# Kernel tuning notes

Hardware: AMD Instinct MI355X
Metric: run time of the kernel (lower is better)

## Reference

```python
import jax, jax.numpy as jnp
import numpy as np

N, E, H, L, G, C = 50000, 800000, 64, 4, 500, 10
BN_EPS = 1e-5


def setup_inputs() -> dict:
    key = jax.random.key(0)
    ks = jax.random.split(key, 24)
    x = jax.random.normal(ks[0], (N, H), dtype=jnp.float32)
    edge_index = jax.random.randint(ks[1], (2, E), 0, N, dtype=jnp.int64)
    batch = jnp.sort(jax.random.randint(ks[2], (N,), 0, G, dtype=jnp.int64))
    s = 1.0 / np.sqrt(H)
    # stacked per-layer GIN MLP params: Linear->BN->ReLU->Linear->BN->ReLU
    conv_W1 = jax.random.uniform(ks[3], (L, H, H), minval=-s, maxval=s, dtype=jnp.float32)
    conv_b1 = jax.random.uniform(ks[4], (L, H), minval=-s, maxval=s, dtype=jnp.float32)
    bn1_g = jax.random.uniform(ks[5], (L, H), minval=0.5, maxval=1.5, dtype=jnp.float32)
    bn1_b = jax.random.normal(ks[6], (L, H), dtype=jnp.float32) * 0.1
    bn1_m = jax.random.normal(ks[7], (L, H), dtype=jnp.float32) * 0.1
    bn1_v = jax.random.uniform(ks[8], (L, H), minval=0.5, maxval=1.5, dtype=jnp.float32)
    conv_W2 = jax.random.uniform(ks[9], (L, H, H), minval=-s, maxval=s, dtype=jnp.float32)
    conv_b2 = jax.random.uniform(ks[10], (L, H), minval=-s, maxval=s, dtype=jnp.float32)
    bn2_g = jax.random.uniform(ks[11], (L, H), minval=0.5, maxval=1.5, dtype=jnp.float32)
    bn2_b = jax.random.normal(ks[12], (L, H), dtype=jnp.float32) * 0.1
    bn2_m = jax.random.normal(ks[13], (L, H), dtype=jnp.float32) * 0.1
    bn2_v = jax.random.uniform(ks[14], (L, H), minval=0.5, maxval=1.5, dtype=jnp.float32)
    s1 = 1.0 / np.sqrt(L * H)
    lin1_W = jax.random.uniform(ks[15], (L * H, H), minval=-s1, maxval=s1, dtype=jnp.float32)
    lin1_b = jax.random.uniform(ks[16], (H,), minval=-s1, maxval=s1, dtype=jnp.float32)
    lin2_W = jax.random.uniform(ks[17], (H, C), minval=-s, maxval=s, dtype=jnp.float32)
    lin2_b = jax.random.uniform(ks[18], (C,), minval=-s, maxval=s, dtype=jnp.float32)
    return dict(x=x, edge_index=edge_index, batch=batch,
                conv_W1=conv_W1, conv_b1=conv_b1, bn1_g=bn1_g, bn1_b=bn1_b, bn1_m=bn1_m, bn1_v=bn1_v,
                conv_W2=conv_W2, conv_b2=conv_b2, bn2_g=bn2_g, bn2_b=bn2_b, bn2_m=bn2_m, bn2_v=bn2_v,
                lin1_W=lin1_W, lin1_b=lin1_b, lin2_W=lin2_W, lin2_b=lin2_b)


def _bn(h, g, b, m, v):
    # eval-mode BatchNorm1d with running stats
    return g * (h - m) * jax.lax.rsqrt(v + BN_EPS) + b


def reference(x, edge_index, batch,
              conv_W1, conv_b1, bn1_g, bn1_b, bn1_m, bn1_v,
              conv_W2, conv_b2, bn2_g, bn2_b, bn2_m, bn2_v,
              lin1_W, lin1_b, lin2_W, lin2_b):
    src, dst = edge_index[0], edge_index[1]

    def layer(h, p):
        W1, b1, g1, be1, m1, v1, W2, b2, g2, be2, m2, v2 = p
        # GIN aggregation (eps=0): h_i + sum_{j->i} h_j, scatter-add over edges
        agg = jax.ops.segment_sum(h[src], dst, num_segments=N)
        z = h + agg
        z = jax.nn.relu(_bn(z @ W1 + b1, g1, be1, m1, v1))
        z = jax.nn.relu(_bn(z @ W2 + b2, g2, be2, m2, v2))
        return z, z

    params = (conv_W1, conv_b1, bn1_g, bn1_b, bn1_m, bn1_v,
              conv_W2, conv_b2, bn2_g, bn2_b, bn2_m, bn2_v)
    _, xs = jax.lax.scan(layer, x, params)          # [L, N, H]
    xcat = jnp.transpose(xs, (1, 0, 2)).reshape(N, L * H)  # JK 'cat'
    pooled = jax.ops.segment_sum(xcat, batch, num_segments=G)  # sum readout [G, L*H]
    h = jax.nn.relu(pooled @ lin1_W + lin1_b)
    # dropout is identity in eval mode
    return h @ lin2_W + lin2_b  # [G, C]
```

## Files before the change

kernel.cpp:

```cpp
#include <hip/hip_runtime.h>

#define NN 50000
#define NE 800000
#define HH 64
#define LL 4
#define GG 500
#define CC 10
#define BN_EPS 1e-5f
#define SCB 200
#define NPART 6250
#define ECHUNK 2048
#define NCHUNK 391

__device__ inline float bf2f(unsigned int u16) {
    union { unsigned int i; float f; } v; v.i = u16 << 16; return v.f;
}
__device__ inline unsigned short f2bf(float f) {
    union { float f; unsigned int i; } v; v.f = f;
    unsigned int u = v.i + 0x7fffu + ((v.i >> 16) & 1u);
    return (unsigned short)(u >> 16);
}
__device__ inline void addrow8(float* acc, uint4 u) {
    #pragma unroll
    for (int q = 0; q < 4; ++q) {
        unsigned int w = (&u.x)[q];
        union { unsigned int i; float f; } lo, hi;
        lo.i = w << 16; hi.i = w & 0xffff0000u;
        acc[2 * q]     += lo.f;
        acc[2 * q + 1] += hi.f;
    }
}

__global__ __launch_bounds__(256) void k_cast(const float* __restrict__ x, unsigned short* __restrict__ xb) {
    int i = blockIdx.x * 256 + threadIdx.x;
    if (i < NN * 16) {
        float4 v = ((const float4*)x)[i];
        uint2 p;
        p.x = (unsigned int)f2bf(v.x) | ((unsigned int)f2bf(v.y) << 16);
        p.y = (unsigned int)f2bf(v.z) | ((unsigned int)f2bf(v.w) << 16);
        ((uint2*)xb)[i] = p;
    }
}

__global__ __launch_bounds__(256) void k_hist8(const int* __restrict__ dst, int* __restrict__ deg) {
    int part  = blockIdx.x & 7;
    int chunk = blockIdx.x >> 3;
    int lo = part * NPART, hi = lo + NPART;
    int base = chunk * ECHUNK + threadIdx.x;
    #pragma unroll
    for (int i = 0; i < 8; ++i) {
        int e = base + i * 256;
        if (e < NE) {
            int d = dst[e];
            if (d >= lo && d < hi) atomicAdd(&deg[d], 1);
        }
    }
}

__global__ __launch_bounds__(256) void k_scan1(const int* __restrict__ deg, int* __restrict__ incl,
                                               int* __restrict__ bsum) {
    int t = threadIdx.x;
    int idx = blockIdx.x * 256 + t;
    __shared__ int s[256];
    int v = (idx < NN) ? deg[idx] : 0;
    s[t] = v;
    __syncthreads();
    for (int off = 1; off < 256; off <<= 1) {
        int u = (t >= off) ? s[t - off] : 0;
        __syncthreads();
        if (t >= off) s[t] += u;
        __syncthreads();
    }
    if (idx < NN) incl[idx] = s[t];
    if (t == 255) bsum[blockIdx.x] = s[255];
}

__global__ __launch_bounds__(256) void k_scan2(const int* __restrict__ bsum, int* __restrict__ boff,
                                               int* __restrict__ row_ptr) {
    int t = threadIdx.x;
    __shared__ int s[256];
    int v = (t < SCB) ? bsum[t] : 0;
    s[t] = v;
    __syncthreads();
    for (int off = 1; off < 256; off <<= 1) {
        int u = (t >= off) ? s[t - off] : 0;
        __syncthreads();
        if (t >= off) s[t] += u;
        __syncthreads();
    }
    if (t < SCB) boff[t] = s[t] - v;
    if (t == 255) row_ptr[NN] = s[255];
}

__global__ __launch_bounds__(256) void k_scan3(const int* __restrict__ deg, const int* __restrict__ incl,
                                               const int* __restrict__ boff, int* __restrict__ row_ptr) {
    int idx = blockIdx.x * 256 + threadIdx.x;
    if (idx < NN) row_ptr[idx] = incl[idx] - deg[idx] + boff[blockIdx.x];
}

__global__ __launch_bounds__(256) void k_scatter8(const int* __restrict__ src, const int* __restrict__ dst,
                                                  const int* __restrict__ row_ptr, int* __restrict__ cursor,
                                                  int* __restrict__ col) {
    int part  = blockIdx.x & 7;
    int chunk = blockIdx.x >> 3;
    int lo = part * NPART, hi = lo + NPART;
    int base = chunk * ECHUNK + threadIdx.x;
    #pragma unroll
    for (int i = 0; i < 8; ++i) {
        int e = base + i * 256;
        if (e < NE) {
            int d = dst[e];
            if (d >= lo && d < hi) {
                int pos = atomicAdd(&cursor[d], 1);
                col[row_ptr[d] + pos] = src[e];
            }
        }
    }
}

__global__ __launch_bounds__(256) void k_agg(
    const unsigned short* __restrict__ hb, unsigned short* __restrict__ aggb,
    const int* __restrict__ row_ptr, const int* __restrict__ col)
{
    int tid  = threadIdx.x;
    int lane = tid & 63;
    int wave = tid >> 6;
    int gl   = lane & 7;
    int grp  = lane >> 3;
    int n = blockIdx.x * 32 + wave * 8 + grp;
    if (n >= NN) return;

    const uint4* hv = (const uint4*)hb;
    float acc[8]  = {0.f, 0.f, 0.f, 0.f, 0.f, 0.f, 0.f, 0.f};
    float acc2[8] = {0.f, 0.f, 0.f, 0.f, 0.f, 0.f, 0.f, 0.f};
    addrow8(acc, hv[(size_t)n * 8 + gl]);

    int j = row_ptr[n], fin = row_ptr[n + 1];
    for (; j + 4 <= fin; j += 4) {
        int s0 = col[j], s1 = col[j + 1], s2 = col[j + 2], s3 = col[j + 3];
        uint4 u0 = hv[(size_t)s0 * 8 + gl];
        uint4 u1 = hv[(size_t)s1 * 8 + gl];
        uint4 u2 = hv[(size_t)s2 * 8 + gl];
        uint4 u3 = hv[(size_t)s3 * 8 + gl];
        addrow8(acc, u0);  addrow8(acc2, u1);
        addrow8(acc, u2);  addrow8(acc2, u3);
    }
    for (; j < fin; ++j)
        addrow8(acc, hv[(size_t)col[j] * 8 + gl]);

    #pragma unroll
    for (int q = 0; q < 8; ++q) acc[q] += acc2[q];

    uint4 o;
    o.x = (unsigned int)f2bf(acc[0]) | ((unsigned int)f2bf(acc[1]) << 16);
    o.y = (unsigned int)f2bf(acc[2]) | ((unsigned int)f2bf(acc[3]) << 16);
    o.z = (unsigned int)f2bf(acc[4]) | ((unsigned int)f2bf(acc[5]) << 16);
    o.w = (unsigned int)f2bf(acc[6]) | ((unsigned int)f2bf(acc[7]) << 16);
    ((uint4*)(aggb + (size_t)n * HH))[gl] = o;
}

#define MT 128
#define SAP 68

__global__ __launch_bounds__(256) void k_mlp2(
    const unsigned short* __restrict__ agg, unsigned short* __restrict__ h_out,
    const int* __restrict__ batch, float* __restrict__ pooled, int layer,
    const float* __restrict__ W1, const float* __restrict__ lb1,
    const float* __restrict__ g1, const float* __restrict__ bb1,
    const float* __restrict__ m1, const float* __restrict__ v1,
    const float* __restrict__ W2, const float* __restrict__ lb2,
    const float* __restrict__ g2, const float* __restrict__ bb2,
    const float* __restrict__ m2, const float* __restrict__ v2)
{
    __shared__ float sW[64 * 64];
    __shared__ float sA[MT * SAP];

    int tid = threadIdx.x;
    int c0  = (tid & 15) * 4;
    int rt  = tid >> 4;
    int base = blockIdx.x * MT;

    float sc1v[4], sh1v[4], sc2v[4], sh2v[4];
    #pragma unroll
    for (int i = 0; i < 4; ++i) {
        int c = c0 + i;
        float s1 = g1[c] * rsqrtf(v1[c] + BN_EPS);
        sc1v[i] = s1;
        sh1v[i] = (lb1[c] - m1[c]) * s1 + bb1[c];
        float s2 = g2[c] * rsqrtf(v2[c] + BN_EPS);
        sc2v[i] = s2;
        sh2v[i] = (lb2[c] - m2[c]) * s2 + bb2[c];
    }

    for (int i = tid; i < 1024; i += 256)
        ((float4*)sW)[i] = ((const float4*)W1)[i];
    for (int i = tid; i < MT * 8; i += 256) {
        int r = i >> 3, cq = i & 7;
        int gr = base + r;
        uint4 u = (gr < NN) ? ((const uint4*)(agg + (size_t)gr * HH))[cq]
                            : make_uint4(0, 0, 0, 0);
        float* dp = &sA[r * SAP + cq * 8];
        dp[0] = bf2f(u.x & 0xffffu); dp[1] = bf2f(u.x >> 16);
        dp[2] = bf2f(u.y & 0xffffu); dp[3] = bf2f(u.y >> 16);
        dp[4] = bf2f(u.z & 0xffffu); dp[5] = bf2f(u.z >> 16);
        dp[6] = bf2f(u.w & 0xffffu); dp[7] = bf2f(u.w >> 16);
    }
    __syncthreads();

    float acc1[8][4];
    #pragma unroll
    for (int i = 0; i < 8; ++i) { acc1[i][0]=0.f; acc1[i][1]=0.f; acc1[i][2]=0.f; acc1[i][3]=0.f; }
    for (int k4 = 0; k4 < 16; ++k4) {
        float4 a[8];
        #pragma unroll
        for (int i = 0; i < 8; ++i)
            a[i] = *(const float4*)&sA[(rt + 16 * i) * SAP + k4 * 4];
        #pragma unroll
        for (int kk = 0; kk < 4; ++kk) {
            float4 w = *(const float4*)&sW[(k4 * 4 + kk) * 64 + c0];
            #pragma unroll
            for (int i = 0; i < 8; ++i) {
                float av = (&a[i].x)[kk];
                acc1[i][0] = fmaf(av, w.x, acc1[i][0]);
                acc1[i][1] = fmaf(av, w.y, acc1[i][1]);
                acc1[i][2] = fmaf(av, w.z, acc1[i][2]);
                acc1[i][3] = fmaf(av, w.w, acc1[i][3]);
            }
        }
    }
    __syncthreads();

    #pragma unroll
    for (int i = 0; i < 8; ++i) {
        float4 z;
        z.x = fmaxf(fmaf(acc1[i][0], sc1v[0], sh1v[0]), 0.f);
        z.y = fmaxf(fmaf(acc1[i][1], sc1v[1], sh1v[1]), 0.f);
        z.z = fmaxf(fmaf(acc1[i][2], sc1v[2], sh1v[2]), 0.f);
        z.w = fmaxf(fmaf(acc1[i][3], sc1v[3], sh1v[3]), 0.f);
        *(float4*)&sA[(rt + 16 * i) * SAP + c0] = z;
    }
    for (int i = tid; i < 1024; i += 256)
        ((float4*)sW)[i] = ((const float4*)W2)[i];
    __syncthreads();

    float acc2[8][4];
    #pragma unroll
    for (int i = 0; i < 8; ++i) { acc2[i][0]=0.f; acc2[i][1]=0.f; acc2[i][2]=0.f; acc2[i][3]=0.f; }
    for (int k4 = 0; k4 < 16; ++k4) {
        float4 a[8];
        #pragma unroll
        for (int i = 0; i < 8; ++i)
            a[i] = *(const float4*)&sA[(rt + 16 * i) * SAP + k4 * 4];
        #pragma unroll
        for (int kk = 0; kk < 4; ++kk) {
            float4 w = *(const float4*)&sW[(k4 * 4 + kk) * 64 + c0];
            #pragma unroll
            for (int i = 0; i < 8; ++i) {
                float av = (&a[i].x)[kk];
                acc2[i][0] = fmaf(av, w.x, acc2[i][0]);
                acc2[i][1] = fmaf(av, w.y, acc2[i][1]);
                acc2[i][2] = fmaf(av, w.z, acc2[i][2]);
                acc2[i][3] = fmaf(av, w.w, acc2[i][3]);
            }
        }
    }
    __syncthreads();

    #pragma unroll
    for (int i = 0; i < 8; ++i) {
        int gr = base + rt + 16 * i;
        float zx = fmaxf(fmaf(acc2[i][0], sc2v[0], sh2v[0]), 0.f);
        float zy = fmaxf(fmaf(acc2[i][1], sc2v[1], sh2v[1]), 0.f);
        float zz = fmaxf(fmaf(acc2[i][2], sc2v[2], sh2v[2]), 0.f);
        float zw = fmaxf(fmaf(acc2[i][3], sc2v[3], sh2v[3]), 0.f);
        *(float4*)&sA[(rt + 16 * i) * SAP + c0] = make_float4(zx, zy, zz, zw);
        if (gr < NN) {
            uint2 p;
            p.x = (unsigned int)f2bf(zx) | ((unsigned int)f2bf(zy) << 16);
            p.y = (unsigned int)f2bf(zz) | ((unsigned int)f2bf(zw) << 16);
            *(uint2*)&h_out[(size_t)gr * HH + c0] = p;
        }
    }
    __syncthreads();

    int thi = base + MT; if (thi > NN) thi = NN;
    int gfirst = batch[base];
    int glast  = batch[thi - 1];
    int c = tid & 63;
    int q = tid >> 6;
    float* red = sW;
    for (int g = gfirst; g <= glast; ++g) {
        int lo = base, hi = thi;
        while (lo < hi) { int mid = (lo + hi) >> 1; if (batch[mid] < g) lo = mid + 1; else hi = mid; }
        int lo_g = lo;
        hi = thi;
        while (lo < hi) { int mid = (lo + hi) >> 1; if (batch[mid] < g + 1) lo = mid + 1; else hi = mid; }
        int hi_g = lo;
        float acc = 0.f;
        for (int r = lo_g + q; r < hi_g; r += 4) acc += sA[(r - base) * SAP + c];
        red[tid] = acc;
        __syncthreads();
        if (tid < 64)
            atomicAdd(&pooled[(size_t)g * (LL * HH) + layer * HH + c],
                      red[c] + red[64 + c] + red[128 + c] + red[192 + c]);
        __syncthreads();
    }
}

__global__ __launch_bounds__(64) void k_mlp(const float* __restrict__ pooled,
                                            const float* __restrict__ w1, const float* __restrict__ b1,
                                            const float* __restrict__ w2, const float* __restrict__ b2,
                                            float* __restrict__ out)
{
    int g = blockIdx.x, c = threadIdx.x;
    __shared__ float hh[64];
    float acc = b1[c];
    const float* p = pooled + g * (LL * HH);
    #pragma unroll 8
    for (int k = 0; k < LL * HH; ++k) acc = fmaf(p[k], w1[k * HH + c], acc);
    hh[c] = fmaxf(acc, 0.f);
    __syncthreads();
    if (c < CC) {
        float o = b2[c];
        #pragma unroll
        for (int k = 0; k < HH; ++k) o = fmaf(hh[k], w2[k * CC + c], o);
        out[g * CC + c] = o;
    }
}

extern "C" void kernel_launch(void* const* d_in, const int* in_sizes, int n_in,
                              void* d_out, int out_size, void* d_ws, size_t ws_size,
                              hipStream_t stream) {
    const float* x    = (const float*)d_in[0];
    const int*   ei   = (const int*)d_in[1];
    const int*   bat  = (const int*)d_in[2];
    const float* cW1  = (const float*)d_in[3];
    const float* cb1  = (const float*)d_in[4];
    const float* g1   = (const float*)d_in[5];
    const float* bb1  = (const float*)d_in[6];
    const float* m1   = (const float*)d_in[7];
    const float* v1   = (const float*)d_in[8];
    const float* cW2  = (const float*)d_in[9];
    const float* cb2  = (const float*)d_in[10];
    const float* g2   = (const float*)d_in[11];
    const float* bb2  = (const float*)d_in[12];
    const float* m2   = (const float*)d_in[13];
    const float* v2   = (const float*)d_in[14];
    const float* l1W  = (const float*)d_in[15];
    const float* l1b  = (const float*)d_in[16];
    const float* l2W  = (const float*)d_in[17];
    const float* l2b  = (const float*)d_in[18];

    const int* srcp = ei;
    const int* dstp = ei + NE;

    char* ws = (char*)d_ws;
    size_t off = 0;
    auto alloc = [&](size_t bytes) -> char* {
        char* p = ws + off;
        off += (bytes + 255) & ~size_t(255);
        return p;
    };
    unsigned short* xb   = (unsigned short*)alloc((size_t)NN * HH * 2);
    unsigned short* hb0  = (unsigned short*)alloc((size_t)NN * HH * 2);
    unsigned short* hb1  = (unsigned short*)alloc((size_t)NN * HH * 2);
    unsigned short* aggb = (unsigned short*)alloc((size_t)NN * HH * 2);
    float* pooled  = (float*)alloc((size_t)GG * LL * HH * sizeof(float));
    int*   row_ptr = (int*)alloc((size_t)(NN + 1) * sizeof(int));
    int*   deg     = (int*)alloc((size_t)NN * sizeof(int));
    int*   incl    = (int*)alloc((size_t)NN * sizeof(int));
    int*   cursor  = (int*)alloc((size_t)NN * sizeof(int));
    int*   colx    = (int*)alloc((size_t)NE * sizeof(int));
    int*   bsum    = (int*)alloc(256 * sizeof(int));
    int*   boff    = (int*)alloc(256 * sizeof(int));

    hipMemsetAsync(deg, 0, (size_t)NN * sizeof(int), stream);
    hipMemsetAsync(cursor, 0, (size_t)NN * sizeof(int), stream);
    hipMemsetAsync(pooled, 0, (size_t)GG * LL * HH * sizeof(float), stream);

    k_hist8<<<8 * NCHUNK, 256, 0, stream>>>(dstp, deg);
    k_cast<<<NN * 16 / 256, 256, 0, stream>>>(x, xb);
    k_scan1<<<SCB, 256, 0, stream>>>(deg, incl, bsum);
    k_scan2<<<1, 256, 0, stream>>>(bsum, boff, row_ptr);
    k_scan3<<<SCB, 256, 0, stream>>>(deg, incl, boff, row_ptr);
    k_scatter8<<<8 * NCHUNK, 256, 0, stream>>>(srcp, dstp, row_ptr, cursor, colx);

    const unsigned short* hin = xb;
    unsigned short* bufs[2] = { hb0, hb1 };
    const int AGG_BLK = (NN + 31) / 32;
    const int MLP_BLK = (NN + MT - 1) / MT;
    for (int l = 0; l < LL; ++l) {
        unsigned short* hout = bufs[l & 1];
        k_agg<<<AGG_BLK, 256, 0, stream>>>(hin, aggb, row_ptr, colx);
        k_mlp2<<<MLP_BLK, 256, 0, stream>>>(aggb, hout, bat, pooled, l,
            cW1 + (size_t)l * HH * HH, cb1 + l * HH,
            g1 + l * HH, bb1 + l * HH, m1 + l * HH, v1 + l * HH,
            cW2 + (size_t)l * HH * HH, cb2 + l * HH,
            g2 + l * HH, bb2 + l * HH, m2 + l * HH, v2 + l * HH);
        hin = hout;
    }

    k_mlp<<<GG, 64, 0, stream>>>(pooled, l1W, l1b, l2W, l2b, (float*)d_out);
}
```

Measured before the change: 347.8 us.

## Replace FP32 FMA MLP with bf16 MFMA using hi/lo split weights

After: 315.1 us. 1.1x faster.

```diff
diff --git a/kernel.cpp b/kernel.cpp
--- a/kernel.cpp
+++ b/kernel.cpp
@@ -12,6 +12,9 @@
 #define ECHUNK 2048
 #define NCHUNK 391
 
+typedef short bf16x8 __attribute__((ext_vector_type(8)));
+typedef float f32x4  __attribute__((ext_vector_type(4)));
+
 __device__ inline float bf2f(unsigned int u16) {
     union { unsigned int i; float f; } v; v.i = u16 << 16; return v.f;
 }
@@ -40,6 +43,30 @@
         p.y = (unsigned int)f2bf(v.z) | ((unsigned int)f2bf(v.w) << 16);
         ((uint2*)xb)[i] = p;
     }
+}
+
+__global__ __launch_bounds__(256) void k_prepw(const float* __restrict__ cW1,
+                                               const float* __restrict__ cW2,
+                                               unsigned short* __restrict__ fragW)
+{
+    int idx = blockIdx.x * 256 + threadIdx.x;
+    if (idx >= LL * 2 * 4 * 2 * 64 * 8) return;
+    int j    = idx & 7;
+    int lane = (idx >> 3) & 63;
+    int kh   = (idx >> 9) & 1;
+    int ct   = (idx >> 10) & 3;
+    int g    = (idx >> 12) & 1;
+    int L    = idx >> 13;
+    int k = kh * 32 + (lane >> 4) * 8 + j;
+    int n = ct * 16 + (lane & 15);
+    const float* W = (g == 0 ? cW1 : cW2) + (size_t)L * HH * HH;
+    float w = W[k * HH + n];
+    unsigned short hi = f2bf(w);
+    unsigned short lo = f2bf(w - bf2f(hi));
+    size_t fhi = ((size_t)L * 32 + ((g * 2 + 0) * 4 + ct) * 2 + kh) * 512 + lane * 8 + j;
+    size_t flo = ((size_t)L * 32 + ((g * 2 + 1) * 4 + ct) * 2 + kh) * 512 + lane * 8 + j;
+    fragW[fhi] = hi;
+    fragW[flo] = lo;
 }
 
 __global__ __launch_bounds__(256) void k_hist8(const int* __restrict__ dst, int* __restrict__ deg) {
@@ -160,145 +187,146 @@
 }
 
 #define MT 128
-#define SAP 68
+#define SAB 80
+#define SOF 68
 
 __global__ __launch_bounds__(256) void k_mlp2(
     const unsigned short* __restrict__ agg, unsigned short* __restrict__ h_out,
     const int* __restrict__ batch, float* __restrict__ pooled, int layer,
-    const float* __restrict__ W1, const float* __restrict__ lb1,
-    const float* __restrict__ g1, const float* __restrict__ bb1,
-    const float* __restrict__ m1, const float* __restrict__ v1,
-    const float* __restrict__ W2, const float* __restrict__ lb2,
-    const float* __restrict__ g2, const float* __restrict__ bb2,
-    const float* __restrict__ m2, const float* __restrict__ v2)
+    const unsigned short* __restrict__ fragW,
+    const float* __restrict__ lb1, const float* __restrict__ g1,
+    const float* __restrict__ bb1, const float* __restrict__ m1, const float* __restrict__ v1,
+    const float* __restrict__ lb2, const float* __restrict__ g2,
+    const float* __restrict__ bb2, const float* __restrict__ m2, const float* __restrict__ v2)
 {
-    __shared__ float sW[64 * 64];
-    __shared__ float sA[MT * SAP];
-
-    int tid = threadIdx.x;
-    int c0  = (tid & 15) * 4;
-    int rt  = tid >> 4;
+    __shared__ unsigned short sHi[128 * SAB];
+    __shared__ unsigned short sLo[128 * SAB];
+    __shared__ float sOut[128 * SOF];
+    __shared__ float red[256];
+
+    int tid  = threadIdx.x;
+    int lane = tid & 63;
+    int wave = tid >> 6;
+    int l15 = lane & 15, l4 = lane >> 4;
     int base = blockIdx.x * MT;
+    int wrow = wave * 32;
 
     float sc1v[4], sh1v[4], sc2v[4], sh2v[4];
     #pragma unroll
-    for (int i = 0; i < 4; ++i) {
-        int c = c0 + i;
+    for (int ct = 0; ct < 4; ++ct) {
+        int c = ct * 16 + l15;
         float s1 = g1[c] * rsqrtf(v1[c] + BN_EPS);
-        sc1v[i] = s1;
-        sh1v[i] = (lb1[c] - m1[c]) * s1 + bb1[c];
+        sc1v[ct] = s1; sh1v[ct] = (lb1[c] - m1[c]) * s1 + bb1[c];
         float s2 = g2[c] * rsqrtf(v2[c] + BN_EPS);
-        sc2v[i] = s2;
-        sh2v[i] = (lb2[c] - m2[c]) * s2 + bb2[c];
-    }
-
-    for (int i = tid; i < 1024; i += 256)
-        ((float4*)sW)[i] = ((const float4*)W1)[i];
-    for (int i = tid; i < MT * 8; i += 256) {
-        int r = i >> 3, cq = i & 7;
+        sc2v[ct] = s2; sh2v[ct] = (lb2[c] - m2[c]) * s2 + bb2[c];
+    }
+
+    for (int i = tid; i < 128 * 8; i += 256) {
+        int r = i >> 3, q = i & 7;
         int gr = base + r;
-        uint4 u = (gr < NN) ? ((const uint4*)(agg + (size_t)gr * HH))[cq]
-                            : make_uint4(0, 0, 0, 0);
-        float* dp = &sA[r * SAP + cq * 8];
-        dp[0] = bf2f(u.x & 0xffffu); dp[1] = bf2f(u.x >> 16);
-        dp[2] = bf2f(u.y & 0xffffu); dp[3] = bf2f(u.y >> 16);
-        dp[4] = bf2f(u.z & 0xffffu); dp[5] = bf2f(u.z >> 16);
-        dp[6] = bf2f(u.w & 0xffffu); dp[7] = bf2f(u.w >> 16);
-    }
-    __syncthreads();
-
-    float acc1[8][4];
-    #pragma unroll
-    for (int i = 0; i < 8; ++i) { acc1[i][0]=0.f; acc1[i][1]=0.f; acc1[i][2]=0.f; acc1[i][3]=0.f; }
-    for (int k4 = 0; k4 < 16; ++k4) {
-        float4 a[8];
-        #pragma unroll
-        for (int i = 0; i < 8; ++i)
-            a[i] = *(const float4*)&sA[(rt + 16 * i) * SAP + k4 * 4];
-        #pragma unroll
-        for (int kk = 0; kk < 4; ++kk) {
-            float4 w = *(const float4*)&sW[(k4 * 4 + kk) * 64 + c0];
+        uint4 u = (gr < NN) ? ((const uint4*)(agg + (size_t)gr * HH))[q] : make_uint4(0, 0, 0, 0);
+        *(uint4*)&sHi[r * SAB + q * 8] = u;
+    }
+    __syncthreads();
+
+    const bf16x8* fwv = (const bf16x8*)fragW + ((size_t)layer * 32) * 64;
+
+    bf16x8 a0[2][2];
+    #pragma unroll
+    for (int rt = 0; rt < 2; ++rt)
+        #pragma unroll
+        for (int kh = 0; kh < 2; ++kh)
+            a0[rt][kh] = *(const bf16x8*)&sHi[(wrow + rt * 16 + l15) * SAB + kh * 32 + l4 * 8];
+
+    f32x4 acc[2][4];
+    #pragma unroll
+    for (int rt = 0; rt < 2; ++rt)
+        #pragma unroll
+        for (int ct = 0; ct < 4; ++ct) {
+            f32x4 c = {0.f, 0.f, 0.f, 0.f};
             #pragma unroll
-            for (int i = 0; i < 8; ++i) {
-                float av = (&a[i].x)[kk];
-                acc1[i][0] = fmaf(av, w.x, acc1[i][0]);
-                acc1[i][1] = fmaf(av, w.y, acc1[i][1]);
-                acc1[i][2] = fmaf(av, w.z, acc1[i][2]);
-                acc1[i][3] = fmaf(av, w.w, acc1[i][3]);
+            for (int kh = 0; kh < 2; ++kh) {
+                c = __builtin_amdgcn_mfma_f32_16x16x32_bf16(a0[rt][kh], fwv[((0 * 4 + ct) * 2 + kh) * 64 + lane], c, 0, 0, 0);
+                c = __builtin_amdgcn_mfma_f32_16x16x32_bf16(a0[rt][kh], fwv[((1 * 4 + ct) * 2 + kh) * 64 + lane], c, 0, 0, 0);
             }
-        }
-    }
-    __syncthreads();
-
-    #pragma unroll
-    for (int i = 0; i < 8; ++i) {
-        float4 z;
-        z.x = fmaxf(fmaf(acc1[i][0], sc1v[0], sh1v[0]), 0.f);
-        z.y = fmaxf(fmaf(acc1[i][1], sc1v[1], sh1v[1]), 0.f);
-        z.z = fmaxf(fmaf(acc1[i][2], sc1v[2], sh1v[2]), 0.f);
-        z.w = fmaxf(fmaf(acc1[i][3], sc1v[3], sh1v[3]), 0.f);
-        *(float4*)&sA[(rt + 16 * i) * SAP + c0] = z;
-    }
-    for (int i = tid; i < 1024; i += 256)
-        ((float4*)sW)[i] = ((const float4*)W2)[i];
-    __syncthreads();
-
-    float acc2[8][4];
-    #pragma unroll
-    for (int i = 0; i < 8; ++i) { acc2[i][0]=0.f; acc2[i][1]=0.f; acc2[i][2]=0.f; acc2[i][3]=0.f; }
-    for (int k4 = 0; k4 < 16; ++k4) {
-        float4 a[8];
-        #pragma unroll
-        for (int i = 0; i < 8; ++i)
-            a[i] = *(const float4*)&sA[(rt + 16 * i) * SAP + k4 * 4];
-        #pragma unroll
-        for (int kk = 0; kk < 4; ++kk) {
-            float4 w = *(const float4*)&sW[(k4 * 4 + kk) * 64 + c0];
+            acc[rt][ct] = c;
+        }
+    __syncthreads();
+
+    #pragma unroll
+    for (int rt = 0; rt < 2; ++rt)
+        #pragma unroll
+        for (int ct = 0; ct < 4; ++ct)
             #pragma unroll
-            for (int i = 0; i < 8; ++i) {
-                float av = (&a[i].x)[kk];
-                acc2[i][0] = fmaf(av, w.x, acc2[i][0]);
-                acc2[i][1] = fmaf(av, w.y, acc2[i][1]);
-                acc2[i][2] = fmaf(av, w.z, acc2[i][2]);
-                acc2[i][3] = fmaf(av, w.w, acc2[i][3]);
+            for (int rg = 0; rg < 4; ++rg) {
+                int r = wrow + rt * 16 + l4 * 4 + rg;
+                float z = fmaxf(fmaf(acc[rt][ct][rg], sc1v[ct], sh1v[ct]), 0.f);
+                unsigned short hi = f2bf(z);
+                sHi[r * SAB + ct * 16 + l15] = hi;
+                sLo[r * SAB + ct * 16 + l15] = f2bf(z - bf2f(hi));
             }
-        }
-    }
-    __syncthreads();
-
-    #pragma unroll
-    for (int i = 0; i < 8; ++i) {
-        int gr = base + rt + 16 * i;
-        float zx = fmaxf(fmaf(acc2[i][0], sc2v[0], sh2v[0]), 0.f);
-        float zy = fmaxf(fmaf(acc2[i][1], sc2v[1], sh2v[1]), 0.f);
-        float zz = fmaxf(fmaf(acc2[i][2], sc2v[2], sh2v[2]), 0.f);
-        float zw = fmaxf(fmaf(acc2[i][3], sc2v[3], sh2v[3]), 0.f);
-        *(float4*)&sA[(rt + 16 * i) * SAP + c0] = make_float4(zx, zy, zz, zw);
+    __syncthreads();
+
+    bf16x8 ah[2][2], al[2][2];
+    #pragma unroll
+    for (int rt = 0; rt < 2; ++rt)
+        #pragma unroll
+        for (int kh = 0; kh < 2; ++kh) {
+            int off = (wrow + rt * 16 + l15) * SAB + kh * 32 + l4 * 8;
+            ah[rt][kh] = *(const bf16x8*)&sHi[off];
+            al[rt][kh] = *(const bf16x8*)&sLo[off];
+        }
+    #pragma unroll
+    for (int rt = 0; rt < 2; ++rt)
+        #pragma unroll
+        for (int ct = 0; ct < 4; ++ct) {
+            f32x4 c = {0.f, 0.f, 0.f, 0.f};
+            #pragma unroll
+            for (int kh = 0; kh < 2; ++kh) {
+                bf16x8 bh = fwv[((2 * 4 + ct) * 2 + kh) * 64 + lane];
+                bf16x8 bl = fwv[((3 * 4 + ct) * 2 + kh) * 64 + lane];
+                c = __builtin_amdgcn_mfma_f32_16x16x32_bf16(ah[rt][kh], bh, c, 0, 0, 0);
+                c = __builtin_amdgcn_mfma_f32_16x16x32_bf16(al[rt][kh], bh, c, 0, 0, 0);
+                c = __builtin_amdgcn_mfma_f32_16x16x32_bf16(ah[rt][kh], bl, c, 0, 0, 0);
+            }
+            #pragma unroll
+            for (int rg = 0; rg < 4; ++rg) {
+                int r = wrow + rt * 16 + l4 * 4 + rg;
+                float z = fmaxf(fmaf(c[rg], sc2v[ct], sh2v[ct]), 0.f);
+                sOut[r * SOF + ct * 16 + l15] = z;
+            }
+        }
+    __syncthreads();
+
+    for (int i = tid; i < 128 * 8; i += 256) {
+        int r = i >> 3, q = i & 7;
+        int gr = base + r;
         if (gr < NN) {
-            uint2 p;
-            p.x = (unsigned int)f2bf(zx) | ((unsigned int)f2bf(zy) << 16);
-            p.y = (unsigned int)f2bf(zz) | ((unsigned int)f2bf(zw) << 16);
-            *(uint2*)&h_out[(size_t)gr * HH + c0] = p;
-        }
-    }
-    __syncthreads();
+            const float* sp = &sOut[r * SOF + q * 8];
+            uint4 o;
+            o.x = (unsigned int)f2bf(sp[0]) | ((unsigned int)f2bf(sp[1]) << 16);
+            o.y = (unsigned int)f2bf(sp[2]) | ((unsigned int)f2bf(sp[3]) << 16);
+            o.z = (unsigned int)f2bf(sp[4]) | ((unsigned int)f2bf(sp[5]) << 16);
+            o.w = (unsigned int)f2bf(sp[6]) | ((unsigned int)f2bf(sp[7]) << 16);
+            ((uint4*)(h_out + (size_t)gr * HH))[q] = o;
+        }
+    }
 
     int thi = base + MT; if (thi > NN) thi = NN;
     int gfirst = batch[base];
     int glast  = batch[thi - 1];
     int c = tid & 63;
     int q = tid >> 6;
-    float* red = sW;
     for (int g = gfirst; g <= glast; ++g) {
-        int lo = base, hi = thi;
-        while (lo < hi) { int mid = (lo + hi) >> 1; if (batch[mid] < g) lo = mid + 1; else hi = mid; }
+        int lo = base, hb = thi;
+        while (lo < hb) { int mid = (lo + hb) >> 1; if (batch[mid] < g) lo = mid + 1; else hb = mid; }
         int lo_g = lo;
-        hi = thi;
-        while (lo < hi) { int mid = (lo + hi) >> 1; if (batch[mid] < g + 1) lo = mid + 1; else hi = mid; }
+        hb = thi;
+        while (lo < hb) { int mid = (lo + hb) >> 1; if (batch[mid] < g + 1) lo = mid + 1; else hb = mid; }
         int hi_g = lo;
-        float acc = 0.f;
-        for (int r = lo_g + q; r < hi_g; r += 4) acc += sA[(r - base) * SAP + c];
-        red[tid] = acc;
+        float a = 0.f;
+        for (int r = lo_g + q; r < hi_g; r += 4) a += sOut[(r - base) * SOF + c];
+        red[tid] = a;
         __syncthreads();
         if (tid < 64)
             atomicAdd(&pooled[(size_t)g * (LL * HH) + layer * HH + c],
@@ -361,10 +389,11 @@
         off += (bytes + 255) & ~size_t(255);
         return p;
     };
-    unsigned short* xb   = (unsigned short*)alloc((size_t)NN * HH * 2);
-    unsigned short* hb0  = (unsigned short*)alloc((size_t)NN * HH * 2);
-    unsigned short* hb1  = (unsigned short*)alloc((size_t)NN * HH * 2);
-    unsigned short* aggb = (unsigned short*)alloc((size_t)NN * HH * 2);
+    unsigned short* xb    = (unsigned short*)alloc((size_t)NN * HH * 2);
+    unsigned short* hb0   = (unsigned short*)alloc((size_t)NN * HH * 2);
+    unsigned short* hb1   = (unsigned short*)alloc((size_t)NN * HH * 2);
+    unsigned short* aggb  = (unsigned short*)alloc((size_t)NN * HH * 2);
+    unsigned short* fragW = (unsigned short*)alloc((size_t)LL * 32 * 512 * 2);
     float* pooled  = (float*)alloc((size_t)GG * LL * HH * sizeof(float));
     int*   row_ptr = (int*)alloc((size_t)(NN + 1) * sizeof(int));
     int*   deg     = (int*)alloc((size_t)NN * sizeof(int));
@@ -380,6 +409,7 @@
 
     k_hist8<<<8 * NCHUNK, 256, 0, stream>>>(dstp, deg);
     k_cast<<<NN * 16 / 256, 256, 0, stream>>>(x, xb);
+    k_prepw<<<128, 256, 0, stream>>>(cW1, cW2, fragW);
     k_scan1<<<SCB, 256, 0, stream>>>(deg, incl, bsum);
     k_scan2<<<1, 256, 0, stream>>>(bsum, boff, row_ptr);
     k_scan3<<<SCB, 256, 0, stream>>>(deg, incl, boff, row_ptr);
@@ -392,11 +422,9 @@
     for (int l = 0; l < LL; ++l) {
         unsigned short* hout = bufs[l & 1];
         k_agg<<<AGG_BLK, 256, 0, stream>>>(hin, aggb, row_ptr, colx);
-        k_mlp2<<<MLP_BLK, 256, 0, stream>>>(aggb, hout, bat, pooled, l,
-            cW1 + (size_t)l * HH * HH, cb1 + l * HH,
-            g1 + l * HH, bb1 + l * HH, m1 + l * HH, v1 + l * HH,
-            cW2 + (size_t)l * HH * HH, cb2 + l * HH,
-            g2 + l * HH, bb2 + l * HH, m2 + l * HH, v2 + l * HH);
+        k_mlp2<<<MLP_BLK, 256, 0, stream>>>(aggb, hout, bat, pooled, l, fragW,
+            cb1 + l * HH, g1 + l * HH, bb1 + l * HH, m1 + l * HH, v1 + l * HH,
+            cb2 + l * HH, g2 + l * HH, bb2 + l * HH, m2 + l * HH, v2 + l * HH);
         hin = hout;
     }
 
```
